# Optimization experiments

Measured on AMD Instinct MI355X. Metric: run time of the kernel, lower is better.

## Reference

```python
import jax, jax.numpy as jnp
import numpy as np

NEG_SLOPE = 0.2

def _gat_layer(x, src, dst, W, a_src, a_dst, b, heads, out_ch, num_nodes):
    # x: [N, F_in] -> h: [N, H, C]
    h = (x @ W).reshape(num_nodes, heads, out_ch)
    alpha_s = jnp.sum(h * a_src, axis=-1)  # [N, H]
    alpha_d = jnp.sum(h * a_dst, axis=-1)  # [N, H]
    e = jax.nn.leaky_relu(alpha_s[src] + alpha_d[dst], NEG_SLOPE)  # [E, H]
    # segment softmax over edges grouped by destination node
    seg_max = jax.ops.segment_max(e, dst, num_segments=num_nodes)
    seg_max = jnp.where(jnp.isfinite(seg_max), seg_max, 0.0)
    e = jnp.exp(e - jax.lax.stop_gradient(seg_max)[dst])
    denom = jax.ops.segment_sum(e, dst, num_segments=num_nodes)
    alpha = e / (denom[dst] + 1e-16)  # [E, H]
    msgs = h[src] * alpha[:, :, None]  # [E, H, C]
    out = jax.ops.segment_sum(msgs, dst, num_segments=num_nodes)  # [N, H, C]
    return out.reshape(num_nodes, heads * out_ch) + b


def setup_inputs() -> dict:
    key = jax.random.key(0)
    ks = jax.random.split(key, 11)
    N, E, F, H, C = 100000, 1600000, 128, 4, 32
    x = jax.random.normal(ks[0], (N, F), dtype=jnp.float32)
    edge_index = jax.random.randint(ks[1], (2, E), 0, N, dtype=jnp.int64)
    s = 0.1
    return {
        "x": x,
        "edge_index": edge_index,
        "W1": jax.random.normal(ks[2], (F, H * C), dtype=jnp.float32) * s,
        "att_src1": jax.random.normal(ks[3], (H, C), dtype=jnp.float32) * s,
        "att_dst1": jax.random.normal(ks[4], (H, C), dtype=jnp.float32) * s,
        "b1": jax.random.normal(ks[5], (H * C,), dtype=jnp.float32) * s,
        "W2": jax.random.normal(ks[6], (H * C, F), dtype=jnp.float32) * s,
        "att_src2": jax.random.normal(ks[7], (1, F), dtype=jnp.float32) * s,
        "att_dst2": jax.random.normal(ks[8], (1, F), dtype=jnp.float32) * s,
        "b2": jax.random.normal(ks[9], (F,), dtype=jnp.float32) * s,
    }


def reference(x, edge_index, W1, att_src1, att_dst1, b1, W2, att_src2, att_dst2, b2):
    N = x.shape[0]
    H, C = att_src1.shape
    F = x.shape[1]
    # PyG GATConv adds self-loops by default
    loop = jnp.arange(N, dtype=edge_index.dtype)
    src = jnp.concatenate([edge_index[0], loop])
    dst = jnp.concatenate([edge_index[1], loop])
    # dropout is identity in eval mode (training=False)
    h = _gat_layer(x, src, dst, W1, att_src1, att_dst1, b1, H, C, N)
    out = _gat_layer(h, src, dst, W2, att_src2, att_dst2, b2, 1, F, N)
    return out
```

## Files before the change

### kernel.cpp

```cpp
#include <hip/hip_runtime.h>
#include <cstdint>
#include <cstddef>

#define NEG_SLOPE 0.2f

typedef __attribute__((ext_vector_type(8))) short short8;
typedef __attribute__((ext_vector_type(4))) float f32x4;

__device__ __forceinline__ float lrelu(float v) { return v > 0.0f ? v : NEG_SLOPE * v; }

__device__ __forceinline__ unsigned short f2bf(float f) {
  unsigned u = __float_as_uint(f);
  unsigned r = (u + 0x7fff + ((u >> 16) & 1)) >> 16;
  return (unsigned short)r;
}
__device__ __forceinline__ float bf2f(unsigned short u) {
  return __uint_as_float((unsigned)u << 16);
}
__device__ __forceinline__ unsigned pack2bf(float a, float b) {
  return (unsigned)f2bf(a) | ((unsigned)f2bf(b) << 16);
}

__device__ __forceinline__ float selh4(float4 v, int h) {
  return (h == 0) ? v.x : (h == 1) ? v.y : (h == 2) ? v.z : v.w;
}

__global__ __launch_bounds__(256) void prep(const float* __restrict__ W1,
                                            const float* __restrict__ W2,
                                            unsigned short* __restrict__ WT1,
                                            unsigned short* __restrict__ WT2,
                                            int* __restrict__ cnt, int N) {
  int i = blockIdx.x * 256 + threadIdx.x;
  if (i < 16384) {
    int n = i >> 7, k = i & 127;
    WT1[i] = f2bf(W1[k * 128 + n]);
  } else if (i < 32768) {
    int j = i - 16384;
    int n = j >> 7, k = j & 127;
    WT2[j] = f2bf(W2[k * 128 + n]);
  }
  if (i < N) cnt[i] = 0;
}

template <int H, bool BF16IN>
__global__ __launch_bounds__(256) void gemm_mfma(const void* __restrict__ Xv,
                                                 const unsigned short* __restrict__ WT,
                                                 unsigned short* __restrict__ Ybf,
                                                 const float* __restrict__ Asrc,
                                                 const float* __restrict__ Adst,
                                                 float* __restrict__ AS,
                                                 float* __restrict__ AD, int N) {
  __shared__ unsigned short xs[64 * 136];
  __shared__ unsigned short wsh[128 * 136];
  __shared__ float ash[128];
  __shared__ float adh[128];
  const int tid = threadIdx.x;
  const int rowBase = blockIdx.x * 64;
  const int rowsHere = min(64, N - rowBase);

  if (tid < 128) ash[tid] = Asrc[tid];
  else adh[tid - 128] = Adst[tid - 128];

#pragma unroll
  for (int it = 0; it < 8; ++it) {
    int idx = it * 256 + tid;
    int n = idx >> 4, k16 = idx & 15;
    *(uint4*)(wsh + n * 136 + k16 * 8) = *(const uint4*)(WT + (size_t)n * 128 + k16 * 8);
  }
  if constexpr (BF16IN) {
    const unsigned short* Xb = (const unsigned short*)Xv;
#pragma unroll
    for (int it = 0; it < 4; ++it) {
      int idx = it * 256 + tid;
      int r = idx >> 4, c8 = idx & 15;
      uint4 v = make_uint4(0, 0, 0, 0);
      if (r < rowsHere) v = *(const uint4*)(Xb + (size_t)(rowBase + r) * 128 + c8 * 8);
      *(uint4*)(xs + r * 136 + c8 * 8) = v;
    }
  } else {
    const float* Xf = (const float*)Xv;
#pragma unroll
    for (int it = 0; it < 8; ++it) {
      int idx = it * 256 + tid;
      int r = idx >> 5, c4 = idx & 31;
      float4 v = make_float4(0.f, 0.f, 0.f, 0.f);
      if (r < rowsHere) v = *(const float4*)(Xf + (size_t)(rowBase + r) * 128 + c4 * 4);
      ushort4 bv;
      bv.x = f2bf(v.x); bv.y = f2bf(v.y); bv.z = f2bf(v.z); bv.w = f2bf(v.w);
      *(ushort4*)(xs + r * 136 + c4 * 4) = bv;
    }
  }
  __syncthreads();

  const int lane = tid & 63;
  const int w = tid >> 6;
  const int m15 = lane & 15;
  const int quad = lane >> 4;
  f32x4 acc[8];
#pragma unroll
  for (int t = 0; t < 8; ++t) acc[t] = (f32x4){0.f, 0.f, 0.f, 0.f};

#pragma unroll
  for (int k0 = 0; k0 < 128; k0 += 32) {
    short8 a = *(const short8*)(xs + (16 * w + m15) * 136 + k0 + quad * 8);
#pragma unroll
    for (int t = 0; t < 8; ++t) {
      short8 b = *(const short8*)(wsh + (t * 16 + m15) * 136 + k0 + quad * 8);
      acc[t] = __builtin_amdgcn_mfma_f32_16x16x32_bf16(a, b, acc[t], 0, 0, 0);
    }
  }

  __syncthreads();
#pragma unroll
  for (int t = 0; t < 8; ++t) {
#pragma unroll
    for (int r = 0; r < 4; ++r) {
      int row = 16 * w + quad * 4 + r;
      xs[row * 136 + t * 16 + m15] = f2bf(acc[t][r]);
    }
  }
  __syncthreads();
#pragma unroll
  for (int it = 0; it < 4; ++it) {
    int idx = it * 256 + tid;
    int r = idx >> 4, c8 = idx & 15;
    if (r < rowsHere)
      *(uint4*)(Ybf + (size_t)(rowBase + r) * 128 + c8 * 8) = *(const uint4*)(xs + r * 136 + c8 * 8);
  }

  {
    const int r = tid >> 2;
    const int part = tid & 3;
    if (r < rowsHere) {
      const unsigned short* hp = xs + r * 136 + part * 32;
      float as = 0.f, ad = 0.f;
#pragma unroll
      for (int c4 = 0; c4 < 4; ++c4) {
        uint4 hw = *(const uint4*)(hp + c4 * 8);
        unsigned wds[4] = {hw.x, hw.y, hw.z, hw.w};
#pragma unroll
        for (int k = 0; k < 4; ++k) {
          const int c = part * 32 + c4 * 8 + k * 2;
          float v0 = bf2f((unsigned short)wds[k]);
          float v1 = bf2f((unsigned short)(wds[k] >> 16));
          as += v0 * ash[c] + v1 * ash[c + 1];
          ad += v0 * adh[c] + v1 * adh[c + 1];
        }
      }
      if (H == 4) {
        AS[(size_t)(rowBase + r) * 4 + part] = as;
        AD[(size_t)(rowBase + r) * 4 + part] = ad;
      } else {
        as += __shfl_xor(as, 1, 4);
        as += __shfl_xor(as, 2, 4);
        ad += __shfl_xor(ad, 1, 4);
        ad += __shfl_xor(ad, 2, 4);
        if (part == 0) { AS[rowBase + r] = as; AD[rowBase + r] = ad; }
      }
    }
  }
}

__global__ __launch_bounds__(256) void csr_count(const int* __restrict__ ei, int E, int Etot,
                                                 int* __restrict__ cnt) {
  int e = blockIdx.x * 256 + threadIdx.x;
  if (e >= Etot) return;
  int d = (e < E) ? ei[E + e] : (e - E);
  atomicAdd(&cnt[d], 1);
}

__global__ __launch_bounds__(256) void scan_blocks(const int* __restrict__ cnt,
                                                   int* __restrict__ rowStart,
                                                   int* __restrict__ blockSums, int N) {
  __shared__ int sh[256];
  const int tid = threadIdx.x;
  const int i = blockIdx.x * 256 + tid;
  int v = (i < N) ? cnt[i] : 0;
  sh[tid] = v;
  __syncthreads();
  for (int o = 1; o < 256; o <<= 1) {
    int t = (tid >= o) ? sh[tid - o] : 0;
    __syncthreads();
    sh[tid] += t;
    __syncthreads();
  }
  if (i < N) rowStart[i] = sh[tid] - v;
  if (tid == 255) blockSums[blockIdx.x] = sh[255];
}

__global__ __launch_bounds__(256) void scan_sums(int* __restrict__ bs, int nb) {
  __shared__ int sh[256];
  __shared__ int carryS;
  const int tid = threadIdx.x;
  if (tid == 0) carryS = 0;
  __syncthreads();
  for (int c = 0; c < nb; c += 256) {
    int i = c + tid;
    int v = (i < nb) ? bs[i] : 0;
    sh[tid] = v;
    __syncthreads();
    for (int o = 1; o < 256; o <<= 1) {
      int t = (tid >= o) ? sh[tid - o] : 0;
      __syncthreads();
      sh[tid] += t;
      __syncthreads();
    }
    int carry = carryS;
    if (i < nb) bs[i] = carry + sh[tid] - v;
    int total = sh[255];
    __syncthreads();
    if (tid == 0) carryS = carry + total;
    __syncthreads();
  }
}

__global__ __launch_bounds__(256) void add_offsets(int* __restrict__ rowStart,
                                                   const int* __restrict__ bs,
                                                   int* __restrict__ cursor, int N, int Etot) {
  int i = blockIdx.x * 256 + threadIdx.x;
  if (i == 0) rowStart[N] = Etot;
  if (i >= N) return;
  int r = rowStart[i] + bs[i >> 8];
  rowStart[i] = r;
  cursor[i] = r;
}

#define SCAT_CHUNK 2048
__global__ __launch_bounds__(256) void csr_scatter_x(const int* __restrict__ ei, int E, int Etot,
                                                     int* __restrict__ cursor,
                                                     int* __restrict__ srcS, int nper) {
  const int xcd = blockIdx.x & 7;
  const int lo = xcd * nper;
  const int hi = lo + nper;
  const int e0 = (blockIdx.x >> 3) * SCAT_CHUNK + threadIdx.x;
#pragma unroll
  for (int it = 0; it < SCAT_CHUNK / 256; ++it) {
    int e = e0 + it * 256;
    if (e < Etot) {
      int d = (e < E) ? ei[E + e] : (e - E);
      if (d >= lo && d < hi) {
        int s = (e < E) ? ei[e] : d;
        int pos = atomicAdd(&cursor[d], 1);
        srcS[pos] = s;
      }
    }
  }
}

template <int H, bool OUTBF>
__global__ __launch_bounds__(256) void gat_node(
    const int* __restrict__ rowStart, const int* __restrict__ srcS,
    const float* __restrict__ AS, const float* __restrict__ AD,
    const unsigned short* __restrict__ Hbf, const float* __restrict__ B,
    void* __restrict__ Out, int N) {
  const int g = threadIdx.x >> 4;
  const int n = blockIdx.x * 16 + g;
  if (n >= N) return;
  const int l = threadIdx.x & 15;
  const int beg = rowStart[n];
  const int end = rowStart[n + 1];
  const int f0 = l * 8;
  const int myh = (H == 4) ? (l >> 2) : 0;

  float4 adv = make_float4(0.f, 0.f, 0.f, 0.f);
  if (H == 4) adv = *(const float4*)(AD + (size_t)n * 4);
  else adv.x = AD[n];

  float4 m = make_float4(-INFINITY, -INFINITY, -INFINITY, -INFINITY);
  for (int i = beg + l; i < end; i += 16) {
    const int s = srcS[i];
    if (H == 4) {
      float4 as = *(const float4*)(AS + (size_t)s * 4);
      m.x = fmaxf(m.x, lrelu(as.x + adv.x));
      m.y = fmaxf(m.y, lrelu(as.y + adv.y));
      m.z = fmaxf(m.z, lrelu(as.z + adv.z));
      m.w = fmaxf(m.w, lrelu(as.w + adv.w));
    } else {
      m.x = fmaxf(m.x, lrelu(AS[s] + adv.x));
    }
  }
#pragma unroll
  for (int o = 8; o >= 1; o >>= 1) {
    m.x = fmaxf(m.x, __shfl_xor(m.x, o, 16));
    if (H == 4) {
      m.y = fmaxf(m.y, __shfl_xor(m.y, o, 16));
      m.z = fmaxf(m.z, __shfl_xor(m.z, o, 16));
      m.w = fmaxf(m.w, __shfl_xor(m.w, o, 16));
    }
  }
  const float m_my  = (H == 4) ? selh4(m, myh)   : m.x;
  const float ad_my = (H == 4) ? selh4(adv, myh) : adv.x;

  float den = 0.f;
  float acc[8];
#pragma unroll
  for (int k = 0; k < 8; ++k) acc[k] = 0.f;

  auto ISSUE = [&](int ib, int (&sj)[8], float (&pv)[8], uint4 (&hv)[8]) {
#pragma unroll
    for (int q = 0; q < 8; ++q) {
      int idx = ib + q;
      sj[q] = srcS[idx < end ? idx : beg];
    }
#pragma unroll
    for (int q = 0; q < 8; ++q)
      hv[q] = *(const uint4*)(Hbf + (size_t)sj[q] * 128 + f0);
#pragma unroll
    for (int q = 0; q < 8; ++q) {
      const float a = (H == 4) ? AS[(size_t)sj[q] * 4 + myh] : AS[sj[q]];
      float p = __expf(lrelu(a + ad_my) - m_my);
      pv[q] = (ib + q < end) ? p : 0.f;
    }
  };
  auto CONSUME = [&](float (&pv)[8], uint4 (&hv)[8]) {
#pragma unroll
    for (int q = 0; q < 8; ++q) {
      const float aj = pv[q];
      den += aj;
      acc[0] += bf2f((unsigned short)hv[q].x) * aj;
      acc[1] += bf2f((unsigned short)(hv[q].x >> 16)) * aj;
      acc[2] += bf2f((unsigned short)hv[q].y) * aj;
      acc[3] += bf2f((unsigned short)(hv[q].y >> 16)) * aj;
      acc[4] += bf2f((unsigned short)hv[q].z) * aj;
      acc[5] += bf2f((unsigned short)(hv[q].z >> 16)) * aj;
      acc[6] += bf2f((unsigned short)hv[q].w) * aj;
      acc[7] += bf2f((unsigned short)(hv[q].w >> 16)) * aj;
    }
  };

  int sjA[8], sjB[8];
  float pvA[8], pvB[8];
  uint4 hvA[8], hvB[8];
  int i = beg;
  ISSUE(i, sjA, pvA, hvA);
  for (;;) {
    int inext = i + 8;
    if (inext < end) ISSUE(inext, sjB, pvB, hvB);
    CONSUME(pvA, hvA);
    i = inext;
    if (i >= end) break;
    inext = i + 8;
    if (inext < end) ISSUE(inext, sjA, pvA, hvA);
    CONSUME(pvB, hvB);
    i = inext;
    if (i >= end) break;
  }

  const float inv = 1.0f / (den + 1e-16f);
  float o[8];
#pragma unroll
  for (int k = 0; k < 8; ++k) o[k] = acc[k] * inv + B[f0 + k];
  if constexpr (OUTBF) {
    uint4 wv;
    wv.x = pack2bf(o[0], o[1]);
    wv.y = pack2bf(o[2], o[3]);
    wv.z = pack2bf(o[4], o[5]);
    wv.w = pack2bf(o[6], o[7]);
    *(uint4*)((unsigned short*)Out + (size_t)n * 128 + f0) = wv;
  } else {
    float* Of = (float*)Out;
    float4 o0, o1;
    o0.x = o[0]; o0.y = o[1]; o0.z = o[2]; o0.w = o[3];
    o1.x = o[4]; o1.y = o[5]; o1.z = o[6]; o1.w = o[7];
    *(float4*)(Of + (size_t)n * 128 + f0) = o0;
    *(float4*)(Of + (size_t)n * 128 + f0 + 4) = o1;
  }
}

extern "C" void kernel_launch(void* const* d_in, const int* in_sizes, int n_in,
                              void* d_out, int out_size, void* d_ws, size_t ws_size,
                              hipStream_t stream) {
  const float* x    = (const float*)d_in[0];
  const int*   ei   = (const int*)d_in[1];
  const float* W1   = (const float*)d_in[2];
  const float* as1w = (const float*)d_in[3];
  const float* ad1w = (const float*)d_in[4];
  const float* b1   = (const float*)d_in[5];
  const float* W2   = (const float*)d_in[6];
  const float* as2w = (const float*)d_in[7];
  const float* ad2w = (const float*)d_in[8];
  const float* b2   = (const float*)d_in[9];

  const int N = in_sizes[0] / 128;
  const int E = in_sizes[1] / 2;
  const int Etot = E + N;
  const int nb = (N + 255) / 256;

  char* ws = (char*)d_ws;
  size_t off = 0;
  auto alloc = [&](size_t bytes) -> void* {
    void* p = ws + off;
    off = (off + bytes + 255) & ~(size_t)255;
    return p;
  };
  unsigned short* Hbf   = (unsigned short*)alloc((size_t)N * 128 * 2);
  unsigned short* out1b = (unsigned short*)alloc((size_t)N * 128 * 2);
  float* AS1  = (float*)alloc((size_t)N * 4 * 4);
  float* AD1  = (float*)alloc((size_t)N * 4 * 4);
  float* AS2  = (float*)alloc((size_t)N * 4);
  float* AD2  = (float*)alloc((size_t)N * 4);
  unsigned short* WT1 = (unsigned short*)alloc(128 * 128 * 2);
  unsigned short* WT2 = (unsigned short*)alloc(128 * 128 * 2);
  int*   cnt      = (int*)alloc((size_t)N * 4);
  int*   rowStart = (int*)alloc((size_t)(N + 1) * 4);
  int*   cursor   = (int*)alloc((size_t)N * 4);
  int*   blockSums= (int*)alloc((size_t)nb * 4);
  int*   srcS     = (int*)alloc((size_t)Etot * 4);

  const int prepBlocks = (max(32768, N) + 255) / 256;
  prep<<<prepBlocks, 256, 0, stream>>>(W1, W2, WT1, WT2, cnt, N);

  const int ebBlocks = (Etot + 255) / 256;
  csr_count<<<ebBlocks, 256, 0, stream>>>(ei, E, Etot, cnt);
  scan_blocks<<<nb, 256, 0, stream>>>(cnt, rowStart, blockSums, N);
  scan_sums<<<1, 256, 0, stream>>>(blockSums, nb);
  add_offsets<<<nb, 256, 0, stream>>>(rowStart, blockSums, cursor, N, Etot);
  const int nper = (N + 7) / 8;
  const int scatBlocks = 8 * ((Etot + SCAT_CHUNK - 1) / SCAT_CHUNK);
  csr_scatter_x<<<scatBlocks, 256, 0, stream>>>(ei, E, Etot, cursor, srcS, nper);

  const int gemmBlocks = (N + 63) / 64;
  const int nodeBlocks = (N + 15) / 16;

  gemm_mfma<4, false><<<gemmBlocks, 256, 0, stream>>>(x, WT1, Hbf, as1w, ad1w, AS1, AD1, N);
  gat_node<4, true><<<nodeBlocks, 256, 0, stream>>>(rowStart, srcS, AS1, AD1, Hbf, b1, out1b, N);

  gemm_mfma<1, true><<<gemmBlocks, 256, 0, stream>>>(out1b, WT2, Hbf, as2w, ad2w, AS2, AD2, N);
  gat_node<1, false><<<nodeBlocks, 256, 0, stream>>>(rowStart, srcS, AS2, AD2, Hbf, b2, d_out, N);
}
```

Measured before the change: 447.1 us.

## Vectorize CSR count/scatter, drop XCD-partitioned scatter, retile GEMM warps by column

The CSR count and scatter kernels now have each thread handle four edges through int4 loads. The scatter no longer launches eight passes over the edge list that filter destinations by XCD range, so it reads the edges once but loses the per-XCD locality of its cursor atomics. Separately, the MFMA GEMM now gives each wave two column tiles across all four row tiles instead of one row tile across eight column tiles. This changes the balance of LDS A and B loads per MFMA.

Measured after the change: 499.6 us. 11.8% more time.

```diff
diff --git a/kernel.cpp b/kernel.cpp
--- a/kernel.cpp
+++ b/kernel.cpp
@@ -96,29 +96,36 @@
   const int w = tid >> 6;
   const int m15 = lane & 15;
   const int quad = lane >> 4;
-  f32x4 acc[8];
-#pragma unroll
-  for (int t = 0; t < 8; ++t) acc[t] = (f32x4){0.f, 0.f, 0.f, 0.f};
+  f32x4 acc[4][2];
+#pragma unroll
+  for (int rt = 0; rt < 4; ++rt)
+#pragma unroll
+    for (int tt = 0; tt < 2; ++tt) acc[rt][tt] = (f32x4){0.f, 0.f, 0.f, 0.f};
 
 #pragma unroll
   for (int k0 = 0; k0 < 128; k0 += 32) {
-    short8 a = *(const short8*)(xs + (16 * w + m15) * 136 + k0 + quad * 8);
-#pragma unroll
-    for (int t = 0; t < 8; ++t) {
-      short8 b = *(const short8*)(wsh + (t * 16 + m15) * 136 + k0 + quad * 8);
-      acc[t] = __builtin_amdgcn_mfma_f32_16x16x32_bf16(a, b, acc[t], 0, 0, 0);
+    short8 b0 = *(const short8*)(wsh + ((2 * w + 0) * 16 + m15) * 136 + k0 + quad * 8);
+    short8 b1 = *(const short8*)(wsh + ((2 * w + 1) * 16 + m15) * 136 + k0 + quad * 8);
+#pragma unroll
+    for (int rt = 0; rt < 4; ++rt) {
+      short8 a = *(const short8*)(xs + (rt * 16 + m15) * 136 + k0 + quad * 8);
+      acc[rt][0] = __builtin_amdgcn_mfma_f32_16x16x32_bf16(a, b0, acc[rt][0], 0, 0, 0);
+      acc[rt][1] = __builtin_amdgcn_mfma_f32_16x16x32_bf16(a, b1, acc[rt][1], 0, 0, 0);
     }
   }
 
   __syncthreads();
 #pragma unroll
-  for (int t = 0; t < 8; ++t) {
-#pragma unroll
-    for (int r = 0; r < 4; ++r) {
-      int row = 16 * w + quad * 4 + r;
-      xs[row * 136 + t * 16 + m15] = f2bf(acc[t][r]);
-    }
-  }
+  for (int rt = 0; rt < 4; ++rt)
+#pragma unroll
+    for (int tt = 0; tt < 2; ++tt) {
+#pragma unroll
+      for (int r = 0; r < 4; ++r) {
+        int row = rt * 16 + quad * 4 + r;
+        int col = (2 * w + tt) * 16 + m15;
+        xs[row * 136 + col] = f2bf(acc[rt][tt][r]);
+      }
+    }
   __syncthreads();
 #pragma unroll
   for (int it = 0; it < 4; ++it) {
@@ -163,10 +170,24 @@
 
 __global__ __launch_bounds__(256) void csr_count(const int* __restrict__ ei, int E, int Etot,
                                                  int* __restrict__ cnt) {
-  int e = blockIdx.x * 256 + threadIdx.x;
-  if (e >= Etot) return;
-  int d = (e < E) ? ei[E + e] : (e - E);
-  atomicAdd(&cnt[d], 1);
+  int e0 = (blockIdx.x * 256 + threadIdx.x) * 4;
+  if (e0 >= Etot) return;
+  if (((E & 3) == 0) && (e0 + 3 < E)) {
+    int4 d4 = *(const int4*)(ei + E + e0);
+    atomicAdd(&cnt[d4.x], 1);
+    atomicAdd(&cnt[d4.y], 1);
+    atomicAdd(&cnt[d4.z], 1);
+    atomicAdd(&cnt[d4.w], 1);
+  } else {
+#pragma unroll
+    for (int q = 0; q < 4; ++q) {
+      int e = e0 + q;
+      if (e < Etot) {
+        int d = (e < E) ? ei[E + e] : (e - E);
+        atomicAdd(&cnt[d], 1);
+      }
+    }
+  }
 }
 
 __global__ __launch_bounds__(256) void scan_blocks(const int* __restrict__ cnt,
@@ -225,20 +246,25 @@
   cursor[i] = r;
 }
 
-#define SCAT_CHUNK 2048
-__global__ __launch_bounds__(256) void csr_scatter_x(const int* __restrict__ ei, int E, int Etot,
-                                                     int* __restrict__ cursor,
-                                                     int* __restrict__ srcS, int nper) {
-  const int xcd = blockIdx.x & 7;
-  const int lo = xcd * nper;
-  const int hi = lo + nper;
-  const int e0 = (blockIdx.x >> 3) * SCAT_CHUNK + threadIdx.x;
-#pragma unroll
-  for (int it = 0; it < SCAT_CHUNK / 256; ++it) {
-    int e = e0 + it * 256;
-    if (e < Etot) {
-      int d = (e < E) ? ei[E + e] : (e - E);
-      if (d >= lo && d < hi) {
+__global__ __launch_bounds__(256) void csr_scatter(const int* __restrict__ ei, int E, int Etot,
+                                                   int* __restrict__ cursor,
+                                                   int* __restrict__ srcS) {
+  int e0 = (blockIdx.x * 256 + threadIdx.x) * 4;
+  if (e0 >= Etot) return;
+  if (((E & 3) == 0) && (e0 + 3 < E)) {
+    int4 d4 = *(const int4*)(ei + E + e0);
+    int4 s4 = *(const int4*)(ei + e0);
+    int pos;
+    pos = atomicAdd(&cursor[d4.x], 1); srcS[pos] = s4.x;
+    pos = atomicAdd(&cursor[d4.y], 1); srcS[pos] = s4.y;
+    pos = atomicAdd(&cursor[d4.z], 1); srcS[pos] = s4.z;
+    pos = atomicAdd(&cursor[d4.w], 1); srcS[pos] = s4.w;
+  } else {
+#pragma unroll
+    for (int q = 0; q < 4; ++q) {
+      int e = e0 + q;
+      if (e < Etot) {
+        int d = (e < E) ? ei[E + e] : (e - E);
         int s = (e < E) ? ei[e] : d;
         int pos = atomicAdd(&cursor[d], 1);
         srcS[pos] = s;
@@ -410,14 +436,12 @@
   const int prepBlocks = (max(32768, N) + 255) / 256;
   prep<<<prepBlocks, 256, 0, stream>>>(W1, W2, WT1, WT2, cnt, N);
 
-  const int ebBlocks = (Etot + 255) / 256;
-  csr_count<<<ebBlocks, 256, 0, stream>>>(ei, E, Etot, cnt);
+  const int e4Blocks = (Etot + 1023) / 1024;
+  csr_count<<<e4Blocks, 256, 0, stream>>>(ei, E, Etot, cnt);
   scan_blocks<<<nb, 256, 0, stream>>>(cnt, rowStart, blockSums, N);
   scan_sums<<<1, 256, 0, stream>>>(blockSums, nb);
   add_offsets<<<nb, 256, 0, stream>>>(rowStart, blockSums, cursor, N, Etot);
-  const int nper = (N + 7) / 8;
-  const int scatBlocks = 8 * ((Etot + SCAT_CHUNK - 1) / SCAT_CHUNK);
-  csr_scatter_x<<<scatBlocks, 256, 0, stream>>>(ei, E, Etot, cursor, srcS, nper);
+  csr_scatter<<<e4Blocks, 256, 0, stream>>>(ei, E, Etot, cursor, srcS);
 
   const int gemmBlocks = (N + 63) / 64;
   const int nodeBlocks = (N + 15) / 16;
```
